# Performance work log

Measured on AMD Instinct MI355X. Metric: run time of the kernel, lower is better.

The kernel has to match this reference:

```python
import jax, jax.numpy as jnp
import numpy as np

H = 512
IN = 512
T = 1024
B = 64


def setup_inputs() -> dict:
    key = jax.random.key(0)
    ks = jax.random.split(key, 17)
    s_in = 1.0 / np.sqrt(IN)
    s_h = 1.0 / np.sqrt(H)
    inp = {"x": jax.random.normal(ks[0], (T, B, IN), dtype=jnp.float32)}
    names = [("Wxf", "bxf", True), ("Whf", "bhf", False),
             ("Wxi", "bxi", True), ("Whi", "bhi", False),
             ("Wxo", "bxo", True), ("Who", "bho", False),
             ("Wxg", "bxg", True), ("Whg", "bhg", False)]
    i = 1
    for wn, bn, is_x in names:
        fan = IN if is_x else H
        s = s_in if is_x else s_h
        inp[wn] = jax.random.uniform(ks[i], (H, fan), minval=-s, maxval=s, dtype=jnp.float32)
        inp[bn] = jax.random.uniform(ks[i + 1], (H,), minval=-s, maxval=s, dtype=jnp.float32)
        i += 2
    return inp


def _lstm(x, Wxf, bxf, Whf, bhf, Wxi, bxi, Whi, bhi,
          Wxo, bxo, Who, bho, Wxg, bxg, Whg, bhg):
    # Stack 8 gate linears into 2 GEMMs (same math, gate order f,i,o,g)
    Wx = jnp.concatenate([Wxf, Wxi, Wxo, Wxg], axis=0)   # (4H, IN)
    Wh = jnp.concatenate([Whf, Whi, Who, Whg], axis=0)   # (4H, H)
    b = jnp.concatenate([bxf, bxi, bxo, bxg]) + jnp.concatenate([bhf, bhi, bho, bhg])
    # Precompute input projections for all timesteps: (T, B, 4H)
    xp = jnp.einsum('tbi,gi->tbg', x, Wx) + b
    h0 = jnp.zeros((x.shape[1], Whf.shape[0]), dtype=x.dtype)
    c0 = jnp.zeros_like(h0)

    def step(carry, xpt):
        h, c = carry
        z = xpt + h @ Wh.T                       # (B, 4H)
        f, i, o, g = jnp.split(z, 4, axis=-1)
        f = jax.nn.sigmoid(f)
        i = jax.nn.sigmoid(i)
        o = jax.nn.sigmoid(o)
        c = f * c + i * jnp.tanh(g)
        h = o * jnp.tanh(c)
        return (h, c), h

    (h, c), h_seq = jax.lax.scan(step, (h0, c0), xp)
    return h_seq, h[None], c[None]


def reference(x, Wxf, bxf, Whf, bhf, Wxi, bxi, Whi, bhi,
              Wxo, bxo, Who, bho, Wxg, bxg, Whg, bhg):
    return _lstm(x, Wxf, bxf, Whf, bhf, Wxi, bxi, Whi, bhi,
                 Wxo, bxo, Who, bho, Wxg, bxg, Whg, bhg)
```

## Files before the change

kernel.cpp:

```cpp
#include <hip/hip_runtime.h>


#define TT 1024
#define BB 64
#define DD 512
#define NWG 32
#define HSEQ ((size_t)TT * BB * DD)
#define EXOFF 4096

typedef _Float16 half8 __attribute__((ext_vector_type(8)));
typedef float f32x4 __attribute__((ext_vector_type(4)));
typedef float f32x2 __attribute__((ext_vector_type(2)));

__device__ __forceinline__ float sigm(float v) { return 1.0f / (1.0f + __expf(-v)); }
__device__ __forceinline__ float tanh_fast(float v) { return 2.0f / (1.0f + __expf(-2.0f * v)) - 1.0f; }

#define CVT8(DST, LO, HI) do { \
    DST[0] = (_Float16)LO[0]; DST[1] = (_Float16)LO[1]; \
    DST[2] = (_Float16)LO[2]; DST[3] = (_Float16)LO[3]; \
    DST[4] = (_Float16)HI[0]; DST[5] = (_Float16)HI[1]; \
    DST[6] = (_Float16)HI[2]; DST[7] = (_Float16)HI[3]; } while (0)

#define MFMA16(A, B, C) __builtin_amdgcn_mfma_f32_16x16x32_f16(A, B, C, 0, 0, 0)

__device__ __forceinline__ void load_ex8(const char* base, f32x4 r[8]) {
    const char* p0 = base;
    const char* p1 = base + 4096;
    const char* p2 = base + 8192;
    const char* p3 = base + 12288;
    const char* p4 = base + 16384;
    const char* p5 = base + 20480;
    const char* p6 = base + 24576;
    const char* p7 = base + 28672;
    f32x4 a0, a1, a2, a3, a4, a5, a6, a7;
    asm volatile(
        "global_load_dwordx4 %0, %8, off sc0 sc1\n\t"
        "global_load_dwordx4 %1, %9, off sc0 sc1\n\t"
        "global_load_dwordx4 %2, %10, off sc0 sc1\n\t"
        "global_load_dwordx4 %3, %11, off sc0 sc1\n\t"
        "global_load_dwordx4 %4, %12, off sc0 sc1\n\t"
        "global_load_dwordx4 %5, %13, off sc0 sc1\n\t"
        "global_load_dwordx4 %6, %14, off sc0 sc1\n\t"
        "global_load_dwordx4 %7, %15, off sc0 sc1\n\t"
        "s_waitcnt vmcnt(0)"
        : "=&v"(a0), "=&v"(a1), "=&v"(a2), "=&v"(a3),
          "=&v"(a4), "=&v"(a5), "=&v"(a6), "=&v"(a7)
        : "v"(p0), "v"(p1), "v"(p2), "v"(p3), "v"(p4), "v"(p5), "v"(p6), "v"(p7)
        : "memory");
    r[0] = a0; r[1] = a1; r[2] = a2; r[3] = a3;
    r[4] = a4; r[5] = a5; r[6] = a6; r[7] = a7;
}

__global__ __launch_bounds__(512, 2) void lstm_persist(
    const float* __restrict__ x,
    const float* __restrict__ Wxf, const float* __restrict__ Whf,
    const float* __restrict__ Wxi, const float* __restrict__ Whi,
    const float* __restrict__ Wxo, const float* __restrict__ Who,
    const float* __restrict__ Wxg, const float* __restrict__ Whg,
    const float* __restrict__ bxf, const float* __restrict__ bhf,
    const float* __restrict__ bxi, const float* __restrict__ bhi,
    const float* __restrict__ bxo, const float* __restrict__ bho,
    const float* __restrict__ bxg, const float* __restrict__ bhg,
    float* __restrict__ out, int* __restrict__ flags, char* __restrict__ ex)
{
    const int wg   = blockIdx.x;
    const int grp  = wg >> 4;
    const int w    = wg & 15;
    const int tid  = threadIdx.x;
    const int wid  = tid >> 6;
    const int lane = tid & 63;
    const int quad = lane >> 4;
    const int l16  = lane & 15;
    const int g    = wid & 3;
    const bool is_h = wid >= 4;
    const int sid  = tid & 255;

    __shared__ _Float16 xlds[32][520];
    __shared__ _Float16 hlds[32][520];
    __shared__ float zx[4][32][34];
    __shared__ float zh[4][32][34];
    __shared__ float c_lds[32][34];
    __shared__ float bias_lds[4][32];

    {
        const int e = tid * 2, b = e >> 5, u = e & 31;
        c_lds[b][u] = 0.0f; c_lds[b][u + 1] = 0.0f;
    }
    if (tid < 128) {
        const int gg = tid >> 5, uu = tid & 31;
        const float* bx = (gg == 0) ? bxf : (gg == 1) ? bxi : (gg == 2) ? bxo : bxg;
        const float* bh = (gg == 0) ? bhf : (gg == 1) ? bhi : (gg == 2) ? bho : bhg;
        bias_lds[gg][uu] = bx[w * 32 + uu] + bh[w * 32 + uu];
    }

    const float* Ws = !is_h
        ? ((g == 0) ? Wxf : (g == 1) ? Wxi : (g == 2) ? Wxo : Wxg)
        : ((g == 0) ? Whf : (g == 1) ? Whi : (g == 2) ? Who : Whg);
    half8 wfrag[2][16];
#pragma unroll
    for (int n = 0; n < 2; ++n)
#pragma unroll
        for (int kc = 0; kc < 16; ++kc) {
            const float* p = Ws + (size_t)(w * 32 + n * 16 + l16) * DD + kc * 32 + quad * 8;
            f32x4 lo = *(const f32x4*)p;
            f32x4 hi = *(const f32x4*)(p + 4);
            half8 f; CVT8(f, lo, hi);
            wfrag[n][kc] = f;
        }

    const float* xbase = x + (size_t)grp * 32 * DD;
    const int*   fb    = flags + grp * 16 + (lane & 15);
    char* exg = ex + ((size_t)grp << 15);

    __syncthreads();

    for (int t = 0; t < TT; ++t) {
        if (is_h) __builtin_amdgcn_s_setprio(1);

        if (!is_h) {
            const float* src = xbase + (size_t)t * BB * DD;
#pragma unroll 4
            for (int i = 0; i < 8; ++i) {
                const int flat = i * 2048 + sid * 8;
                const int r = flat >> 9, c = flat & 511;
                const float* p = src + (size_t)r * DD + c;
                f32x4 lo = *(const f32x4*)p;
                f32x4 hi = *(const f32x4*)(p + 4);
                half8 v; CVT8(v, lo, hi);
                *(half8*)&xlds[r][c] = v;
            }
        } else if (t > 0) {
            for (;;) {
                int f;
                asm volatile("global_load_dword %0, %1, off sc0 sc1\n\ts_waitcnt vmcnt(0)"
                             : "=&v"(f) : "v"(fb) : "memory");
                if (__all(f >= t)) break;
                __builtin_amdgcn_s_sleep(1);
            }
            const char* src = exg + (((t & 1) ^ 1) << 16) + sid * 16;
            f32x4 rr[8];
            load_ex8(src, rr);
#pragma unroll
            for (int i = 0; i < 8; ++i) {
                const int flat = i * 2048 + sid * 8;
                const int r = flat >> 9, c = flat & 511;
                union { f32x4 f; half8 h; } u; u.f = rr[i];
                *(half8*)&hlds[r][c] = u.h;
            }
        }
        __syncthreads();

        f32x4 acc00 = {0.f, 0.f, 0.f, 0.f}, acc01 = {0.f, 0.f, 0.f, 0.f};
        f32x4 acc10 = {0.f, 0.f, 0.f, 0.f}, acc11 = {0.f, 0.f, 0.f, 0.f};
        if (!is_h || t > 0) {
            const _Float16 (*alds)[520] = is_h ? hlds : xlds;
#pragma unroll
            for (int kc = 0; kc < 16; ++kc) {
                half8 a0 = *(const half8*)&alds[l16][kc * 32 + quad * 8];
                half8 a1 = *(const half8*)&alds[16 + l16][kc * 32 + quad * 8];
                acc00 = MFMA16(a0, wfrag[0][kc], acc00);
                acc01 = MFMA16(a0, wfrag[1][kc], acc01);
                acc10 = MFMA16(a1, wfrag[0][kc], acc10);
                acc11 = MFMA16(a1, wfrag[1][kc], acc11);
            }
        }
        {
            float (*zb)[34] = is_h ? zh[g] : zx[g];
#pragma unroll
            for (int i = 0; i < 4; ++i) {
                zb[quad * 4 + i][l16]           = acc00[i];
                zb[quad * 4 + i][16 + l16]      = acc01[i];
                zb[16 + quad * 4 + i][l16]      = acc10[i];
                zb[16 + quad * 4 + i][16 + l16] = acc11[i];
            }
        }
        if (is_h) __builtin_amdgcn_s_setprio(0);
        __syncthreads();

        {
            const int e = tid * 2, b = e >> 5, u = e & 31;
            float h2[2];
#pragma unroll
            for (int k = 0; k < 2; ++k) {
                const int uu = u + k;
                float zf = bias_lds[0][uu] + zx[0][b][uu] + zh[0][b][uu];
                float zi = bias_lds[1][uu] + zx[1][b][uu] + zh[1][b][uu];
                float zo = bias_lds[2][uu] + zx[2][b][uu] + zh[2][b][uu];
                float zg = bias_lds[3][uu] + zx[3][b][uu] + zh[3][b][uu];
                float c  = sigm(zf) * c_lds[b][uu] + sigm(zi) * tanh_fast(zg);
                c_lds[b][uu] = c;
                h2[k] = sigm(zo) * tanh_fast(c);
            }
            float* hp = out + (size_t)t * BB * DD + (size_t)(grp * 32 + b) * DD + w * 32 + u;
            *(f32x2*)hp = (f32x2){h2[0], h2[1]};
            if (t == TT - 1) {
                float* fp2 = out + HSEQ + (size_t)(grp * 32 + b) * DD + w * 32 + u;
                fp2[0] = h2[0]; fp2[1] = h2[1];
            }
            union { _Float16 h[2]; unsigned u32; } pk;
            pk.h[0] = (_Float16)h2[0]; pk.h[1] = (_Float16)h2[1];
            char* dst = exg + ((t & 1) << 16)
                      + ((size_t)b * 512 + (w * 32 + u)) * 2;
            asm volatile("global_store_dword %0, %1, off sc0 sc1"
                         :: "v"(dst), "v"(pk.u32) : "memory");
        }
        asm volatile("s_waitcnt vmcnt(0)" ::: "memory");
        __syncthreads();
        if (tid == 0) {
            int val = t + 1;
            int* fp = flags + grp * 16 + w;
            asm volatile("global_store_dword %0, %1, off sc0 sc1"
                         :: "v"(fp), "v"(val) : "memory");
        }
    }

    {
        const int e = tid * 2, b = e >> 5, u = e & 31;
        float* cp = out + HSEQ + (size_t)BB * DD + (size_t)(grp * 32 + b) * DD + w * 32 + u;
        cp[0] = c_lds[b][u];
        cp[1] = c_lds[b][u + 1];
    }
}

extern "C" void kernel_launch(void* const* d_in, const int* in_sizes, int n_in,
                              void* d_out, int out_size, void* d_ws, size_t ws_size,
                              hipStream_t stream) {
    const float* x   = (const float*)d_in[0];
    const float* Wxf = (const float*)d_in[1];  const float* bxf = (const float*)d_in[2];
    const float* Whf = (const float*)d_in[3];  const float* bhf = (const float*)d_in[4];
    const float* Wxi = (const float*)d_in[5];  const float* bxi = (const float*)d_in[6];
    const float* Whi = (const float*)d_in[7];  const float* bhi = (const float*)d_in[8];
    const float* Wxo = (const float*)d_in[9];  const float* bxo = (const float*)d_in[10];
    const float* Who = (const float*)d_in[11]; const float* bho = (const float*)d_in[12];
    const float* Wxg = (const float*)d_in[13]; const float* bxg = (const float*)d_in[14];
    const float* Whg = (const float*)d_in[15]; const float* bhg = (const float*)d_in[16];
    float* out = (float*)d_out;
    int* flags = (int*)d_ws;
    char* ex = (char*)d_ws + EXOFF;

    hipMemsetAsync(d_ws, 0, (size_t)NWG * sizeof(int), stream);

    void* args[] = { &x,
                     &Wxf, &Whf, &Wxi, &Whi, &Wxo, &Who, &Wxg, &Whg,
                     &bxf, &bhf, &bxi, &bhi, &bxo, &bho, &bxg, &bhg,
                     &out, &flags, &ex };
    hipLaunchCooperativeKernel((const void*)lstm_persist,
                               dim3(NWG), dim3(512), args, 0, stream);
}
```

Before: 5.028 ms.

## Prefetch next-step input projection while waiting for recurrent hidden state

The x-projection waves now compute the input GEMM for timestep t+1 during step t, double-buffering its result in LDS, so it leaves the recurrent critical path. They also read x straight from global memory into MFMA fragments instead of staging it through an LDS tile, which drops the xlds buffer. This adds an extra barrier per step and a prologue for step 0. The x work overlaps the flag spin-wait and h-exchange, but the h GEMM now runs after a barrier that also waits on the x waves.

```diff
diff --git a/kernel.cpp b/kernel.cpp
--- a/kernel.cpp
+++ b/kernel.cpp
@@ -75,9 +75,8 @@
     const bool is_h = wid >= 4;
     const int sid  = tid & 255;
 
-    __shared__ _Float16 xlds[32][520];
     __shared__ _Float16 hlds[32][520];
-    __shared__ float zx[4][32][34];
+    __shared__ float zx[2][4][32][34];
     __shared__ float zh[4][32][34];
     __shared__ float c_lds[32][34];
     __shared__ float bias_lds[4][32];
@@ -86,6 +85,7 @@
         const int e = tid * 2, b = e >> 5, u = e & 31;
         c_lds[b][u] = 0.0f; c_lds[b][u + 1] = 0.0f;
     }
+    for (int i = tid; i < 4 * 32 * 34; i += 512) (&zh[0][0][0])[i] = 0.0f;
     if (tid < 128) {
         const int gg = tid >> 5, uu = tid & 31;
         const float* bx = (gg == 0) ? bxf : (gg == 1) ? bxi : (gg == 2) ? bxo : bxg;
@@ -114,58 +114,72 @@
 
     __syncthreads();
 
+    if (!is_h) {
+        const float* pa0 = xbase + (size_t)l16 * DD + quad * 8;
+        const float* pa1 = pa0 + 16 * DD;
+        f32x4 acc00 = {0,0,0,0}, acc01 = {0,0,0,0}, acc10 = {0,0,0,0}, acc11 = {0,0,0,0};
+#pragma unroll
+        for (int kc = 0; kc < 16; ++kc) {
+            f32x4 a0lo = *(const f32x4*)(pa0 + kc * 32);
+            f32x4 a0hi = *(const f32x4*)(pa0 + kc * 32 + 4);
+            f32x4 a1lo = *(const f32x4*)(pa1 + kc * 32);
+            f32x4 a1hi = *(const f32x4*)(pa1 + kc * 32 + 4);
+            half8 a0, a1; CVT8(a0, a0lo, a0hi); CVT8(a1, a1lo, a1hi);
+            acc00 = MFMA16(a0, wfrag[0][kc], acc00);
+            acc01 = MFMA16(a0, wfrag[1][kc], acc01);
+            acc10 = MFMA16(a1, wfrag[0][kc], acc10);
+            acc11 = MFMA16(a1, wfrag[1][kc], acc11);
+        }
+#pragma unroll
+        for (int i = 0; i < 4; ++i) {
+            zx[0][g][quad * 4 + i][l16]           = acc00[i];
+            zx[0][g][quad * 4 + i][16 + l16]      = acc01[i];
+            zx[0][g][16 + quad * 4 + i][l16]      = acc10[i];
+            zx[0][g][16 + quad * 4 + i][16 + l16] = acc11[i];
+        }
+    }
+    __syncthreads();
+
     for (int t = 0; t < TT; ++t) {
-        if (is_h) __builtin_amdgcn_s_setprio(1);
-
-        if (!is_h) {
-            const float* src = xbase + (size_t)t * BB * DD;
-#pragma unroll 4
-            for (int i = 0; i < 8; ++i) {
-                const int flat = i * 2048 + sid * 8;
-                const int r = flat >> 9, c = flat & 511;
-                const float* p = src + (size_t)r * DD + c;
-                f32x4 lo = *(const f32x4*)p;
-                f32x4 hi = *(const f32x4*)(p + 4);
-                half8 v; CVT8(v, lo, hi);
-                *(half8*)&xlds[r][c] = v;
-            }
-        } else if (t > 0) {
-            for (;;) {
-                int f;
-                asm volatile("global_load_dword %0, %1, off sc0 sc1\n\ts_waitcnt vmcnt(0)"
-                             : "=&v"(f) : "v"(fb) : "memory");
-                if (__all(f >= t)) break;
-                __builtin_amdgcn_s_sleep(1);
-            }
-            const char* src = exg + (((t & 1) ^ 1) << 16) + sid * 16;
-            f32x4 rr[8];
-            load_ex8(src, rr);
-#pragma unroll
-            for (int i = 0; i < 8; ++i) {
-                const int flat = i * 2048 + sid * 8;
-                const int r = flat >> 9, c = flat & 511;
-                union { f32x4 f; half8 h; } u; u.f = rr[i];
-                *(half8*)&hlds[r][c] = u.h;
-            }
-        }
-        __syncthreads();
-
-        f32x4 acc00 = {0.f, 0.f, 0.f, 0.f}, acc01 = {0.f, 0.f, 0.f, 0.f};
-        f32x4 acc10 = {0.f, 0.f, 0.f, 0.f}, acc11 = {0.f, 0.f, 0.f, 0.f};
-        if (!is_h || t > 0) {
-            const _Float16 (*alds)[520] = is_h ? hlds : xlds;
+        if (is_h) {
+            __builtin_amdgcn_s_setprio(1);
+            if (t > 0) {
+                for (;;) {
+                    int f;
+                    asm volatile("global_load_dword %0, %1, off sc0 sc1\n\ts_waitcnt vmcnt(0)"
+                                 : "=&v"(f) : "v"(fb) : "memory");
+                    if (__all(f >= t)) break;
+                    __builtin_amdgcn_s_sleep(1);
+                }
+                const char* src = exg + (((t & 1) ^ 1) << 16) + sid * 16;
+                f32x4 rr[8];
+                load_ex8(src, rr);
+#pragma unroll
+                for (int i = 0; i < 8; ++i) {
+                    const int flat = i * 2048 + sid * 8;
+                    const int r = flat >> 9, c = flat & 511;
+                    union { f32x4 f; half8 h; } u; u.f = rr[i];
+                    *(half8*)&hlds[r][c] = u.h;
+                }
+            }
+        } else if (t + 1 < TT) {
+            const float* src = xbase + (size_t)(t + 1) * BB * DD;
+            const float* pa0 = src + (size_t)l16 * DD + quad * 8;
+            const float* pa1 = pa0 + 16 * DD;
+            f32x4 acc00 = {0,0,0,0}, acc01 = {0,0,0,0}, acc10 = {0,0,0,0}, acc11 = {0,0,0,0};
 #pragma unroll
             for (int kc = 0; kc < 16; ++kc) {
-                half8 a0 = *(const half8*)&alds[l16][kc * 32 + quad * 8];
-                half8 a1 = *(const half8*)&alds[16 + l16][kc * 32 + quad * 8];
+                f32x4 a0lo = *(const f32x4*)(pa0 + kc * 32);
+                f32x4 a0hi = *(const f32x4*)(pa0 + kc * 32 + 4);
+                f32x4 a1lo = *(const f32x4*)(pa1 + kc * 32);
+                f32x4 a1hi = *(const f32x4*)(pa1 + kc * 32 + 4);
+                half8 a0, a1; CVT8(a0, a0lo, a0hi); CVT8(a1, a1lo, a1hi);
                 acc00 = MFMA16(a0, wfrag[0][kc], acc00);
                 acc01 = MFMA16(a0, wfrag[1][kc], acc01);
                 acc10 = MFMA16(a1, wfrag[0][kc], acc10);
                 acc11 = MFMA16(a1, wfrag[1][kc], acc11);
             }
-        }
-        {
-            float (*zb)[34] = is_h ? zh[g] : zx[g];
+            float (*zb)[34] = zx[(t + 1) & 1][g];
 #pragma unroll
             for (int i = 0; i < 4; ++i) {
                 zb[quad * 4 + i][l16]           = acc00[i];
@@ -174,19 +188,41 @@
                 zb[16 + quad * 4 + i][16 + l16] = acc11[i];
             }
         }
+        __syncthreads();
+
+        if (is_h && t > 0) {
+            f32x4 acc00 = {0,0,0,0}, acc01 = {0,0,0,0}, acc10 = {0,0,0,0}, acc11 = {0,0,0,0};
+#pragma unroll
+            for (int kc = 0; kc < 16; ++kc) {
+                half8 a0 = *(const half8*)&hlds[l16][kc * 32 + quad * 8];
+                half8 a1 = *(const half8*)&hlds[16 + l16][kc * 32 + quad * 8];
+                acc00 = MFMA16(a0, wfrag[0][kc], acc00);
+                acc01 = MFMA16(a0, wfrag[1][kc], acc01);
+                acc10 = MFMA16(a1, wfrag[0][kc], acc10);
+                acc11 = MFMA16(a1, wfrag[1][kc], acc11);
+            }
+#pragma unroll
+            for (int i = 0; i < 4; ++i) {
+                zh[g][quad * 4 + i][l16]           = acc00[i];
+                zh[g][quad * 4 + i][16 + l16]      = acc01[i];
+                zh[g][16 + quad * 4 + i][l16]      = acc10[i];
+                zh[g][16 + quad * 4 + i][16 + l16] = acc11[i];
+            }
+        }
         if (is_h) __builtin_amdgcn_s_setprio(0);
         __syncthreads();
 
         {
             const int e = tid * 2, b = e >> 5, u = e & 31;
+            const float (*zxp)[32][34] = zx[t & 1];
             float h2[2];
 #pragma unroll
             for (int k = 0; k < 2; ++k) {
                 const int uu = u + k;
-                float zf = bias_lds[0][uu] + zx[0][b][uu] + zh[0][b][uu];
-                float zi = bias_lds[1][uu] + zx[1][b][uu] + zh[1][b][uu];
-                float zo = bias_lds[2][uu] + zx[2][b][uu] + zh[2][b][uu];
-                float zg = bias_lds[3][uu] + zx[3][b][uu] + zh[3][b][uu];
+                float zf = bias_lds[0][uu] + zxp[0][b][uu] + zh[0][b][uu];
+                float zi = bias_lds[1][uu] + zxp[1][b][uu] + zh[1][b][uu];
+                float zo = bias_lds[2][uu] + zxp[2][b][uu] + zh[2][b][uu];
+                float zg = bias_lds[3][uu] + zxp[3][b][uu] + zh[3][b][uu];
                 float c  = sigm(zf) * c_lds[b][uu] + sigm(zi) * tanh_fast(zg);
                 c_lds[b][uu] = c;
                 h2[k] = sigm(zo) * tanh_fast(c);
```

Measured after the change: 12.69 ms. +152.3%, slower.
